# Kernel optimization log

Measured on AMD Instinct MI355X. Metric: run time of the kernel, lower is better.

The kernel has to match this reference:

```python
import jax, jax.numpy as jnp
import numpy as np

B, N, C, H = 8, 1024, 768, 12
D = C // H  # 64


def setup_inputs() -> dict:
    key = jax.random.key(0)
    ks = jax.random.split(key, 6)
    x = jax.random.normal(ks[0], (B, N, C), dtype=jnp.float32)
    pad_mask = jnp.ones((B, N), dtype=jnp.int32)
    # params (torch Linear stored transposed; here kept as (in, out) for x @ W)
    s = 1.0 / np.sqrt(C)
    w_attn = jax.random.uniform(ks[1], (C, 3 * C), jnp.float32, -s, s)
    b_attn = jax.random.uniform(ks[2], (3 * C,), jnp.float32, -s, s)
    w_proj = jax.random.uniform(ks[3], (C, C), jnp.float32, -s, s)
    b_proj = jax.random.uniform(ks[4], (C,), jnp.float32, -s, s)
    return {"x": x, "pad_mask": pad_mask, "w_attn": w_attn,
            "b_attn": b_attn, "w_proj": w_proj, "b_proj": b_proj}


def reference(x, pad_mask, w_attn, b_attn, w_proj, b_proj):
    # qkv projection
    qkv = x @ w_attn + b_attn                      # [B,N,3C]
    q, k, v = jnp.split(qkv, 3, axis=-1)
    q = q.reshape(B, N, H, D).transpose(0, 2, 1, 3)  # [B,H,N,D]
    k = k.reshape(B, N, H, D).transpose(0, 2, 1, 3)
    v = v.reshape(B, N, H, D).transpose(0, 2, 1, 3)
    scale = 1.0 / np.sqrt(D)
    att = jnp.einsum('bhqd,bhkd->bhqk', q, k) * scale  # [B,H,N,N]
    # NOTE: original code's causal masked_fill is non-in-place and discarded,
    # so the causal mask is NOT applied. Only the pad mask (over query rows) is.
    pm = pad_mask.reshape(B, 1, N, 1)
    att = jnp.where(pm == 0, -jnp.inf, att)
    att = jax.nn.softmax(att, axis=-1)
    out = jnp.einsum('bhqk,bhkd->bhqd', att, v)     # [B,H,N,D]
    out = out.transpose(0, 2, 1, 3).reshape(B, N, C)
    # dropout layers are identity in eval mode
    return out @ w_proj + b_proj
```

## Files before the change

kernel.cpp:

```cpp
#include <hip/hip_runtime.h>
#include <hip/hip_bf16.h>

#define B_  8
#define N_  1024
#define C_  768
#define H_  12
#define D_  64
#define C3  2304
#define C2  1536

typedef unsigned short ushort_t;
typedef __attribute__((ext_vector_type(8))) short bf16x8;
typedef __attribute__((ext_vector_type(4))) float f32x4;
typedef __attribute__((ext_vector_type(4))) unsigned int u32x4;

__device__ __forceinline__ ushort_t f2bf(float f) {
    union { float f; unsigned int i; } v;
    v.f = f;
    unsigned int x = v.i;
    if ((x & 0x7f800000u) == 0x7f800000u && (x & 0x007fffffu))
        return (ushort_t)((x >> 16) | 0x0040u);
    return (ushort_t)((x + 0x7fffu + ((x >> 16) & 1u)) >> 16);
}

__device__ __forceinline__ void st1(float* p, float v) { *p = v; }
__device__ __forceinline__ void st1(ushort_t* p, float v) { *p = f2bf(v); }

#define NCVT 6144
#define NTA  1728
#define NTP  576

__device__ __forceinline__ void transpose_tile(
    const float* __restrict__ W, ushort_t* __restrict__ WT,
    int K, int Nn, int n0, int k0, float (*t)[33], int tid)
{
    const int tx = tid & 31, ty = tid >> 5;
    #pragma unroll
    for (int i = 0; i < 4; ++i) {
        const int k = ty + i * 8;
        t[k][tx] = W[(size_t)(k0 + k) * Nn + n0 + tx];
    }
    __syncthreads();
    #pragma unroll
    for (int i = 0; i < 4; ++i) {
        const int n = ty + i * 8;
        WT[(size_t)(n0 + n) * K + k0 + tx] = f2bf(t[tx][n]);
    }
}

__global__ __launch_bounds__(256) void prep(
    const float* __restrict__ X, ushort_t* __restrict__ Y,
    const float* __restrict__ Wa, ushort_t* __restrict__ WaT,
    const float* __restrict__ Wp, ushort_t* __restrict__ WpT)
{
    __shared__ float t[32][33];
    const int bid = blockIdx.x;
    const int tid = threadIdx.x;
    if (bid < NCVT) {
        const int i = (bid * 256 + tid) * 4;
        float4 f = *reinterpret_cast<const float4*>(X + i);
        ushort4 o;
        o.x = f2bf(f.x); o.y = f2bf(f.y); o.z = f2bf(f.z); o.w = f2bf(f.w);
        *reinterpret_cast<ushort4*>(Y + i) = o;
    } else if (bid < NCVT + NTA) {
        const int tt = bid - NCVT;
        transpose_tile(Wa, WaT, C_, C3, (tt % (C3 / 32)) * 32,
                       (tt / (C3 / 32)) * 32, t, tid);
    } else {
        const int tt = bid - NCVT - NTA;
        transpose_tile(Wp, WpT, C_, C_, (tt % (C_ / 32)) * 32,
                       (tt / (C_ / 32)) * 32, t, tid);
    }
}

#define GBK 64

__device__ __forceinline__ void gld_lds16(const ushort_t* g, ushort_t* lds) {
    __builtin_amdgcn_global_load_lds(
        (const __attribute__((address_space(1))) void*)g,
        (__attribute__((address_space(3))) void*)lds, 16, 0, 0);
}

#define G1_NBX   18
#define G1_NBLK  576
#define G1_STEPS 12
#define G1_BUFSZ 24576

__global__ __launch_bounds__(512) void gemm1_mfma(
    const ushort_t* __restrict__ A, const ushort_t* __restrict__ BT,
    const float* __restrict__ bias, ushort_t* __restrict__ Y,
    ushort_t* __restrict__ vtOut)
{
    extern __shared__ ushort_t LDSbuf[];

    const int tid  = threadIdx.x;
    const int wave = tid >> 6;
    const int lane = tid & 63;

    const int hwid = blockIdx.x;
    const int wid  = (hwid & 7) * (G1_NBLK >> 3) + (hwid >> 3);
    const int row0 = (wid / G1_NBX) * 256;
    const int col0 = (wid % G1_NBX) * 128;

    const int wr   = (wave >> 1) * 64;
    const int wc   = (wave & 1) * 64;
    const int l15  = lane & 15;
    const int quad = lane >> 4;
    const int l7   = l15 & 7;

    const int srow = lane >> 3;
    const int sg   = (lane & 7) ^ srow;

    f32x4 acc[4][4] = {};

    auto stage = [&](int buf, int k0) {
        ushort_t* lds = LDSbuf + buf * G1_BUFSZ;
        #pragma unroll
        for (int it = 0; it < 4; ++it) {
            const int baseRow = it * 64 + wave * 8;
            gld_lds16(&A[(size_t)(row0 + baseRow + srow) * C_ + k0 + sg * 8],
                      &lds[baseRow * 64]);
        }
        #pragma unroll
        for (int it = 0; it < 2; ++it) {
            const int baseRow = it * 64 + wave * 8;
            gld_lds16(&BT[(size_t)(col0 + baseRow + srow) * C_ + k0 + sg * 8],
                      &lds[16384 + baseRow * 64]);
        }
    };

    stage(0, 0);
    stage(1, GBK);
    asm volatile("s_waitcnt vmcnt(6)" ::: "memory");
    __builtin_amdgcn_s_barrier();
    __builtin_amdgcn_sched_barrier(0);

    for (int t = 0; t < G1_STEPS; ++t) {
        const ushort_t* const As = LDSbuf + (t % 3) * G1_BUFSZ;
        const ushort_t* const Bs = As + 16384;

        if (t + 2 < G1_STEPS) stage((t + 2) % 3, (t + 2) * GBK);

        #pragma unroll
        for (int kc = 0; kc < 2; ++kc) {
            bf16x8 af[4], bf[4];
            #pragma unroll
            for (int i = 0; i < 4; ++i) {
                const int aslot = (kc * 4 + quad) ^ l7;
                af[i] = *reinterpret_cast<const bf16x8*>(
                    &As[(wr + i * 16 + l15) * 64 + aslot * 8]);
                bf[i] = *reinterpret_cast<const bf16x8*>(
                    &Bs[(wc + i * 16 + l15) * 64 + aslot * 8]);
            }
            #pragma unroll
            for (int i = 0; i < 4; ++i)
                #pragma unroll
                for (int j = 0; j < 4; ++j)
                    acc[i][j] = __builtin_amdgcn_mfma_f32_16x16x32_bf16(
                        af[i], bf[j], acc[i][j], 0, 0, 0);
        }

        if (t + 2 < G1_STEPS)
            asm volatile("s_waitcnt vmcnt(6)" ::: "memory");
        else if (t + 1 < G1_STEPS)
            asm volatile("s_waitcnt vmcnt(0)" ::: "memory");
        __builtin_amdgcn_s_barrier();
        __builtin_amdgcn_sched_barrier(0);
    }

    const float qs = ((col0 + wc) < C_) ? 0.1803368801f : 1.0f;

    if (col0 >= C2) {
        #pragma unroll
        for (int i = 0; i < 4; ++i) {
            const int r0 = row0 + wr + i * 16 + quad * 4;
            const int bb = r0 >> 10;
            const int n  = r0 & 1023;
            const int np = (n & 0x3E0) | (quad << 3) | ((i & 1) << 2);
            #pragma unroll
            for (int j = 0; j < 4; ++j) {
                const int c  = col0 + wc + j * 16 + l15;
                const int cv = c - C2;
                const int hh = cv >> 6, d = cv & 63;
                const float bv = bias[c];
                ushort4 o;
                o.x = f2bf(acc[i][j][0] + bv);
                o.y = f2bf(acc[i][j][1] + bv);
                o.z = f2bf(acc[i][j][2] + bv);
                o.w = f2bf(acc[i][j][3] + bv);
                *reinterpret_cast<ushort4*>(
                    &vtOut[((size_t)(bb * H_ + hh) * D_ + d) * N_ + np]) = o;
            }
        }
    } else {
        #pragma unroll
        for (int i = 0; i < 4; ++i) {
            const int r = row0 + wr + i * 16 + quad * 4;
            #pragma unroll
            for (int j = 0; j < 4; ++j) {
                const int c = col0 + wc + j * 16 + l15;
                const float bv = bias[c];
                #pragma unroll
                for (int t = 0; t < 4; ++t)
                    Y[(size_t)(r + t) * C2 + c] = f2bf((acc[i][j][t] + bv) * qs);
            }
        }
    }
}

template<typename TO, bool SCALEQ>
__global__ __launch_bounds__(256) void gemm_mfma(
    const ushort_t* __restrict__ A, const ushort_t* __restrict__ BT,
    const float* __restrict__ bias, TO* __restrict__ Y, int ldY,
    ushort_t* __restrict__ vtOut, int M, int K, int Nn)
{
    __shared__ ushort_t AB[2][2 * 128 * GBK];

    const int tid  = threadIdx.x;
    const int wave = tid >> 6;
    const int lane = tid & 63;

    const int nbx  = Nn / 128;
    const int nblk = nbx * (M / 128);
    const int hwid = blockIdx.y * gridDim.x + blockIdx.x;
    const int wid  = (hwid & 7) * (nblk >> 3) + (hwid >> 3);
    const int row0 = (wid / nbx) * 128;
    const int col0 = (wid % nbx) * 128;

    const int wr   = (wave >> 1) * 64;
    const int wc   = (wave & 1) * 64;
    const int l15  = lane & 15;
    const int quad = lane >> 4;
    const int l7   = l15 & 7;

    const int srow = lane >> 3;
    const int sg   = (lane & 7) ^ srow;

    f32x4 acc[4][4] = {};

    #pragma unroll
    for (int it = 0; it < 4; ++it) {
        const int baseRow = wave * 32 + it * 8;
        const int r = baseRow + srow;
        gld_lds16(&A [(size_t)(row0 + r) * K + sg * 8], &AB[0][baseRow * GBK]);
        gld_lds16(&BT[(size_t)(col0 + r) * K + sg * 8],
                  &AB[0][128 * GBK + baseRow * GBK]);
    }
    __syncthreads();

    const int nsteps = K / GBK;
    for (int t = 0; t < nsteps; ++t) {
        const int buf = t & 1;
        const ushort_t* const As = AB[buf];
        const ushort_t* const Bs = AB[buf] + 128 * GBK;

        if (t + 1 < nsteps) {
            const int k0 = (t + 1) * GBK;
            #pragma unroll
            for (int it = 0; it < 4; ++it) {
                const int baseRow = wave * 32 + it * 8;
                const int r = baseRow + srow;
                gld_lds16(&A [(size_t)(row0 + r) * K + k0 + sg * 8],
                          &AB[buf ^ 1][baseRow * GBK]);
                gld_lds16(&BT[(size_t)(col0 + r) * K + k0 + sg * 8],
                          &AB[buf ^ 1][128 * GBK + baseRow * GBK]);
            }
        }

        #pragma unroll
        for (int kc = 0; kc < 2; ++kc) {
            bf16x8 af[4], bf[4];
            #pragma unroll
            for (int i = 0; i < 4; ++i) {
                const int aslot = (kc * 4 + quad) ^ l7;
                af[i] = *reinterpret_cast<const bf16x8*>(
                    &As[(wr + i * 16 + l15) * GBK + aslot * 8]);
                bf[i] = *reinterpret_cast<const bf16x8*>(
                    &Bs[(wc + i * 16 + l15) * GBK + aslot * 8]);
            }
            #pragma unroll
            for (int i = 0; i < 4; ++i)
                #pragma unroll
                for (int j = 0; j < 4; ++j)
                    acc[i][j] = __builtin_amdgcn_mfma_f32_16x16x32_bf16(
                        af[i], bf[j], acc[i][j], 0, 0, 0);
        }
        __syncthreads();
    }

    const float qs = (SCALEQ && (col0 + wc) < C_) ? 0.1803368801f : 1.0f;

    if (vtOut != nullptr && col0 >= C2) {
        #pragma unroll
        for (int i = 0; i < 4; ++i) {
            const int r0 = row0 + wr + i * 16 + quad * 4;
            const int bb = r0 >> 10;
            const int n  = r0 & 1023;
            const int np = (n & 0x3E0) | (quad << 3) | ((i & 1) << 2);
            #pragma unroll
            for (int j = 0; j < 4; ++j) {
                const int c  = col0 + wc + j * 16 + l15;
                const int cv = c - C2;
                const int hh = cv >> 6, d = cv & 63;
                const float bv = bias[c];
                ushort4 o;
                o.x = f2bf(acc[i][j][0] + bv);
                o.y = f2bf(acc[i][j][1] + bv);
                o.z = f2bf(acc[i][j][2] + bv);
                o.w = f2bf(acc[i][j][3] + bv);
                *reinterpret_cast<ushort4*>(
                    &vtOut[((size_t)(bb * H_ + hh) * D_ + d) * N_ + np]) = o;
            }
        }
    } else {
        #pragma unroll
        for (int i = 0; i < 4; ++i) {
            const int r = row0 + wr + i * 16 + quad * 4;
            #pragma unroll
            for (int j = 0; j < 4; ++j) {
                const int c = col0 + wc + j * 16 + l15;
                const float bv = bias[c];
                #pragma unroll
                for (int t = 0; t < 4; ++t)
                    st1(&Y[(size_t)(r + t) * ldY + c], (acc[i][j][t] + bv) * qs);
            }
        }
    }
}

__global__ __launch_bounds__(256) void attn_mfma(
    const ushort_t* __restrict__ qk, const ushort_t* __restrict__ vt,
    const int* __restrict__ pad_mask, ushort_t* __restrict__ y)
{
    __shared__ __align__(16) ushort_t KV[2][2 * 64 * 64];

    const int tid  = threadIdx.x;
    const int wave = tid >> 6;
    const int lane = tid & 63;
    const int l15  = lane & 15;
    const int quad = lane >> 4;
    const int l7   = l15 & 7;

    const int wid = (blockIdx.x & 7) * 96 + (blockIdx.x >> 3);
    const int qt = wid & 7;
    const int hb = wid >> 3;
    const int h  = hb % H_;
    const int b  = hb / H_;
    const int q0 = qt * 128 + wave * 32;

    const ushort_t* qkB = qk + (size_t)b * N_ * C2;
    const ushort_t* vtB = vt + ((size_t)(b * H_ + h)) * D_ * N_;
    const int ho = h * D_;

    bf16x8 qf[2][2];
    #pragma unroll
    for (int rt = 0; rt < 2; ++rt)
        #pragma unroll
        for (int kc = 0; kc < 2; ++kc)
            qf[rt][kc] = *reinterpret_cast<const bf16x8*>(
                &qkB[(size_t)(q0 + rt * 16 + l15) * C2 + ho + kc * 32 + quad * 8]);

    int mrow[2][4];
    #pragma unroll
    for (int rt = 0; rt < 2; ++rt)
        #pragma unroll
        for (int t = 0; t < 4; ++t)
            mrow[rt][t] = pad_mask[b * N_ + q0 + rt * 16 + quad * 4 + t];

    f32x4 oacc[2][4] = {};
    float den[2] = {};

    const int srow = lane >> 3;
    const int sg   = (lane & 7) ^ srow;

    #pragma unroll
    for (int it = 0; it < 2; ++it) {
        const int base = wave * 16 + it * 8;
        const int r = base + srow;
        gld_lds16(&qkB[(size_t)r * C2 + C_ + ho + sg * 8], &KV[0][base * 64]);
        gld_lds16(&vtB[(size_t)r * N_ + sg * 8], &KV[0][4096 + base * 64]);
    }
    __syncthreads();

    for (int t = 0; t < N_ / 64; ++t) {
        const int buf = t & 1;
        const ushort_t* const Ks  = KV[buf];
        const ushort_t* const Vts = KV[buf] + 4096;

        if (t + 1 < N_ / 64) {
            const int k0 = (t + 1) * 64;
            #pragma unroll
            for (int it = 0; it < 2; ++it) {
                const int base = wave * 16 + it * 8;
                const int r = base + srow;
                gld_lds16(&qkB[(size_t)(k0 + r) * C2 + C_ + ho + sg * 8],
                          &KV[buf ^ 1][base * 64]);
                gld_lds16(&vtB[(size_t)r * N_ + k0 + sg * 8],
                          &KV[buf ^ 1][4096 + base * 64]);
            }
        }

        f32x4 s[2][4] = {};
        #pragma unroll
        for (int kc = 0; kc < 2; ++kc) {
            bf16x8 kf[4];
            #pragma unroll
            for (int ct = 0; ct < 4; ++ct) {
                const int slot = (kc * 4 + quad) ^ l7;
                kf[ct] = *reinterpret_cast<const bf16x8*>(
                    &Ks[(ct * 16 + l15) * 64 + slot * 8]);
            }
            __builtin_amdgcn_s_setprio(1);
            #pragma unroll
            for (int rt = 0; rt < 2; ++rt)
                #pragma unroll
                for (int ct = 0; ct < 4; ++ct)
                    s[rt][ct] = __builtin_amdgcn_mfma_f32_16x16x32_bf16(
                        kf[ct], qf[rt][kc], s[rt][ct], 0, 0, 0);
            __builtin_amdgcn_s_setprio(0);
        }

        unsigned pk[2][4][2];
        #pragma unroll
        for (int rt = 0; rt < 2; ++rt)
            #pragma unroll
            for (int ct = 0; ct < 4; ++ct) {
                const float p0 = __builtin_amdgcn_exp2f(s[rt][ct][0]);
                const float p1 = __builtin_amdgcn_exp2f(s[rt][ct][1]);
                const float p2 = __builtin_amdgcn_exp2f(s[rt][ct][2]);
                const float p3 = __builtin_amdgcn_exp2f(s[rt][ct][3]);
                den[rt] += (p0 + p1) + (p2 + p3);
                const unsigned x0 = __float_as_uint(p0) + 0x8000u;
                const unsigned x1 = __float_as_uint(p1) + 0x8000u;
                const unsigned x2 = __float_as_uint(p2) + 0x8000u;
                const unsigned x3 = __float_as_uint(p3) + 0x8000u;
                pk[rt][ct][0] = (x0 >> 16) | (x1 & 0xffff0000u);
                pk[rt][ct][1] = (x2 >> 16) | (x3 & 0xffff0000u);
            }

        #pragma unroll
        for (int kc = 0; kc < 2; ++kc) {
            bf16x8 pf[2], vf[4];
            #pragma unroll
            for (int rt = 0; rt < 2; ++rt) {
                const u32x4 pw = (u32x4){pk[rt][kc * 2][0], pk[rt][kc * 2][1],
                                         pk[rt][kc * 2 + 1][0],
                                         pk[rt][kc * 2 + 1][1]};
                pf[rt] = __builtin_bit_cast(bf16x8, pw);
            }
            #pragma unroll
            for (int dt = 0; dt < 4; ++dt) {
                const int slot = (kc * 4 + quad) ^ l7;
                vf[dt] = *reinterpret_cast<const bf16x8*>(
                    &Vts[(dt * 16 + l15) * 64 + slot * 8]);
            }
            __builtin_amdgcn_s_setprio(1);
            #pragma unroll
            for (int rt = 0; rt < 2; ++rt)
                #pragma unroll
                for (int dt = 0; dt < 4; ++dt)
                    oacc[rt][dt] = __builtin_amdgcn_mfma_f32_16x16x32_bf16(
                        pf[rt], vf[dt], oacc[rt][dt], 0, 0, 0);
            __builtin_amdgcn_s_setprio(0);
        }
        __syncthreads();
    }

    ushort_t* const scratch = KV[0] + wave * 32 * 64;

    #pragma unroll
    for (int rt = 0; rt < 2; ++rt) {
        float v = den[rt];
        v += __shfl_xor(v, 16);
        v += __shfl_xor(v, 32);
        den[rt] = v;
    }
    #pragma unroll
    for (int rt = 0; rt < 2; ++rt)
        #pragma unroll
        for (int t = 0; t < 4; ++t) {
            const float dv  = __shfl(den[rt], quad * 4 + t);
            const float inv = mrow[rt][t] ? 1.0f / dv : __builtin_nanf("");
            const int row = rt * 16 + quad * 4 + t;
            #pragma unroll
            for (int dt = 0; dt < 4; ++dt) {
                const int slot = (dt * 2 + (l15 >> 3)) ^ (row & 7);
                scratch[row * 64 + slot * 8 + l7] =
                    f2bf(oacc[rt][dt][t] * inv);
            }
        }
    __syncthreads();
    {
        const int orow = lane >> 1;
        const int og   = (lane & 1) * 4;
        const size_t gr = (size_t)(b * N_ + q0 + orow) * C_ + ho;
        #pragma unroll
        for (int i2 = 0; i2 < 4; ++i2) {
            const int g = og + i2;
            uint4 w = *reinterpret_cast<const uint4*>(
                &scratch[orow * 64 + (g ^ (orow & 7)) * 8]);
            *reinterpret_cast<uint4*>(&y[gr + g * 8]) = w;
        }
    }
}

extern "C" void kernel_launch(void* const* d_in, const int* in_sizes, int n_in,
                              void* d_out, int out_size, void* d_ws, size_t ws_size,
                              hipStream_t stream)
{
    const float* x      = (const float*)d_in[0];
    const int*   pad    = (const int*)d_in[1];
    const float* w_attn = (const float*)d_in[2];
    const float* b_attn = (const float*)d_in[3];
    const float* w_proj = (const float*)d_in[4];
    const float* b_proj = (const float*)d_in[5];
    float* out = (float*)d_out;

    ushort_t* qkb = (ushort_t*)d_ws;
    ushort_t* vtb = qkb + (size_t)B_ * N_ * C2;
    ushort_t* y   = vtb + (size_t)B_ * H_ * D_ * N_;
    ushort_t* xb  = y;
    ushort_t* wat = y + (size_t)B_ * N_ * C_;
    ushort_t* wpt = wat + (size_t)C3 * C_;

    const int M = B_ * N_;

    static bool attr_set = false;
    if (!attr_set) {
        hipFuncSetAttribute(reinterpret_cast<const void*>(&gemm1_mfma),
                            hipFuncAttributeMaxDynamicSharedMemorySize,
                            3 * G1_BUFSZ * 2);
        attr_set = true;
    }

    prep<<<dim3(NCVT + NTA + NTP), dim3(256), 0, stream>>>(
        x, xb, w_attn, wat, w_proj, wpt);

    gemm1_mfma<<<dim3(G1_NBLK), dim3(512), 3 * G1_BUFSZ * 2, stream>>>(
        xb, wat, b_attn, qkb, vtb);

    attn_mfma<<<dim3(B_ * H_ * 8), dim3(256), 0, stream>>>(qkb, vtb, pad, y);

    gemm_mfma<float, false><<<dim3(C_ / 128, M / 128), dim3(256), 0, stream>>>(
        y, wpt, b_proj, out, C_, nullptr, M, C_, C_);
}
```

Before: 188.0 us.

## Fuse fp32-to-bf16 conversion of x into the QKV GEMM A-tile load

The separate pass that converted x to bf16 in the prep kernel is removed. The QKV GEMM now reads fp32 x directly into registers, converts it to bf16 and writes it to LDS, while the weight tiles still use direct global-to-LDS loads. The GEMM is also restructured from a 256x128 tile with 512 threads and a triple-buffered dynamic LDS to a 128x128 tile with 256 threads and static double buffering. This saves a full round trip of the activation through memory and one kernel's worth of work. In exchange the GEMM reads twice the A bytes and repeats them across column blocks, and it has a shallower load pipeline with extra conversion ALU work in the main loop.

```diff
diff --git a/kernel.cpp b/kernel.cpp
--- a/kernel.cpp
+++ b/kernel.cpp
@@ -26,7 +26,6 @@
 __device__ __forceinline__ void st1(float* p, float v) { *p = v; }
 __device__ __forceinline__ void st1(ushort_t* p, float v) { *p = f2bf(v); }
 
-#define NCVT 6144
 #define NTA  1728
 #define NTP  576
 
@@ -49,25 +48,17 @@
 }
 
 __global__ __launch_bounds__(256) void prep(
-    const float* __restrict__ X, ushort_t* __restrict__ Y,
     const float* __restrict__ Wa, ushort_t* __restrict__ WaT,
     const float* __restrict__ Wp, ushort_t* __restrict__ WpT)
 {
     __shared__ float t[32][33];
     const int bid = blockIdx.x;
     const int tid = threadIdx.x;
-    if (bid < NCVT) {
-        const int i = (bid * 256 + tid) * 4;
-        float4 f = *reinterpret_cast<const float4*>(X + i);
-        ushort4 o;
-        o.x = f2bf(f.x); o.y = f2bf(f.y); o.z = f2bf(f.z); o.w = f2bf(f.w);
-        *reinterpret_cast<ushort4*>(Y + i) = o;
-    } else if (bid < NCVT + NTA) {
-        const int tt = bid - NCVT;
-        transpose_tile(Wa, WaT, C_, C3, (tt % (C3 / 32)) * 32,
-                       (tt / (C3 / 32)) * 32, t, tid);
+    if (bid < NTA) {
+        transpose_tile(Wa, WaT, C_, C3, (bid % (C3 / 32)) * 32,
+                       (bid / (C3 / 32)) * 32, t, tid);
     } else {
-        const int tt = bid - NCVT - NTA;
+        const int tt = bid - NTA;
         transpose_tile(Wp, WpT, C_, C_, (tt % (C_ / 32)) * 32,
                        (tt / (C_ / 32)) * 32, t, tid);
     }
@@ -81,26 +72,23 @@
         (__attribute__((address_space(3))) void*)lds, 16, 0, 0);
 }
 
-#define G1_NBX   18
-#define G1_NBLK  576
-#define G1_STEPS 12
-#define G1_BUFSZ 24576
-
-__global__ __launch_bounds__(512) void gemm1_mfma(
-    const ushort_t* __restrict__ A, const ushort_t* __restrict__ BT,
+__global__ __launch_bounds__(256) void gemm1_fused(
+    const float* __restrict__ Ax, const ushort_t* __restrict__ BT,
     const float* __restrict__ bias, ushort_t* __restrict__ Y,
     ushort_t* __restrict__ vtOut)
 {
-    extern __shared__ ushort_t LDSbuf[];
+    __shared__ ushort_t AB[2][2 * 128 * GBK];
 
     const int tid  = threadIdx.x;
     const int wave = tid >> 6;
     const int lane = tid & 63;
 
+    const int nbx  = C3 / 128;
+    const int nblk = nbx * (B_ * N_ / 128);
     const int hwid = blockIdx.x;
-    const int wid  = (hwid & 7) * (G1_NBLK >> 3) + (hwid >> 3);
-    const int row0 = (wid / G1_NBX) * 256;
-    const int col0 = (wid % G1_NBX) * 128;
+    const int wid  = (hwid & 7) * (nblk >> 3) + (hwid >> 3);
+    const int row0 = (wid / nbx) * 128;
+    const int col0 = (wid % nbx) * 128;
 
     const int wr   = (wave >> 1) * 64;
     const int wc   = (wave & 1) * 64;
@@ -112,34 +100,56 @@
     const int sg   = (lane & 7) ^ srow;
 
     f32x4 acc[4][4] = {};
-
-    auto stage = [&](int buf, int k0) {
-        ushort_t* lds = LDSbuf + buf * G1_BUFSZ;
+    float4 areg[4][2];
+
+    auto loadA = [&](int k0) {
         #pragma unroll
         for (int it = 0; it < 4; ++it) {
-            const int baseRow = it * 64 + wave * 8;
-            gld_lds16(&A[(size_t)(row0 + baseRow + srow) * C_ + k0 + sg * 8],
-                      &lds[baseRow * 64]);
-        }
-        #pragma unroll
-        for (int it = 0; it < 2; ++it) {
-            const int baseRow = it * 64 + wave * 8;
+            const int r = wave * 32 + it * 8 + srow;
+            const float* src = &Ax[(size_t)(row0 + r) * C_ + k0 + sg * 8];
+            areg[it][0] = *reinterpret_cast<const float4*>(src);
+            areg[it][1] = *reinterpret_cast<const float4*>(src + 4);
+        }
+    };
+    auto writeA = [&](int buf) {
+        #pragma unroll
+        for (int it = 0; it < 4; ++it) {
+            const int r = wave * 32 + it * 8 + srow;
+            const float4 f0 = areg[it][0];
+            const float4 f1 = areg[it][1];
+            u32x4 pw;
+            pw[0] = (unsigned)f2bf(f0.x) | ((unsigned)f2bf(f0.y) << 16);
+            pw[1] = (unsigned)f2bf(f0.z) | ((unsigned)f2bf(f0.w) << 16);
+            pw[2] = (unsigned)f2bf(f1.x) | ((unsigned)f2bf(f1.y) << 16);
+            pw[3] = (unsigned)f2bf(f1.z) | ((unsigned)f2bf(f1.w) << 16);
+            *reinterpret_cast<u32x4*>(
+                &AB[buf][r * GBK + (lane & 7) * 8]) = pw;
+        }
+    };
+    auto stageB = [&](int buf, int k0) {
+        #pragma unroll
+        for (int it = 0; it < 4; ++it) {
+            const int baseRow = wave * 32 + it * 8;
             gld_lds16(&BT[(size_t)(col0 + baseRow + srow) * C_ + k0 + sg * 8],
-                      &lds[16384 + baseRow * 64]);
+                      &AB[buf][128 * GBK + baseRow * GBK]);
         }
     };
 
-    stage(0, 0);
-    stage(1, GBK);
-    asm volatile("s_waitcnt vmcnt(6)" ::: "memory");
-    __builtin_amdgcn_s_barrier();
-    __builtin_amdgcn_sched_barrier(0);
-
-    for (int t = 0; t < G1_STEPS; ++t) {
-        const ushort_t* const As = LDSbuf + (t % 3) * G1_BUFSZ;
-        const ushort_t* const Bs = As + 16384;
-
-        if (t + 2 < G1_STEPS) stage((t + 2) % 3, (t + 2) * GBK);
+    loadA(0);
+    stageB(0, 0);
+    writeA(0);
+    __syncthreads();
+
+    const int nsteps = C_ / GBK;
+    for (int t = 0; t < nsteps; ++t) {
+        const int buf = t & 1;
+        const ushort_t* const As = AB[buf];
+        const ushort_t* const Bs = AB[buf] + 128 * GBK;
+
+        if (t + 1 < nsteps) {
+            loadA((t + 1) * GBK);
+            stageB(buf ^ 1, (t + 1) * GBK);
+        }
 
         #pragma unroll
         for (int kc = 0; kc < 2; ++kc) {
@@ -148,9 +158,9 @@
             for (int i = 0; i < 4; ++i) {
                 const int aslot = (kc * 4 + quad) ^ l7;
                 af[i] = *reinterpret_cast<const bf16x8*>(
-                    &As[(wr + i * 16 + l15) * 64 + aslot * 8]);
+                    &As[(wr + i * 16 + l15) * GBK + aslot * 8]);
                 bf[i] = *reinterpret_cast<const bf16x8*>(
-                    &Bs[(wc + i * 16 + l15) * 64 + aslot * 8]);
+                    &Bs[(wc + i * 16 + l15) * GBK + aslot * 8]);
             }
             #pragma unroll
             for (int i = 0; i < 4; ++i)
@@ -160,12 +170,8 @@
                         af[i], bf[j], acc[i][j], 0, 0, 0);
         }
 
-        if (t + 2 < G1_STEPS)
-            asm volatile("s_waitcnt vmcnt(6)" ::: "memory");
-        else if (t + 1 < G1_STEPS)
-            asm volatile("s_waitcnt vmcnt(0)" ::: "memory");
-        __builtin_amdgcn_s_barrier();
-        __builtin_amdgcn_sched_barrier(0);
+        if (t + 1 < nsteps) writeA(buf ^ 1);
+        __syncthreads();
     }
 
     const float qs = ((col0 + wc) < C_) ? 0.1803368801f : 1.0f;
@@ -519,25 +525,15 @@
     ushort_t* qkb = (ushort_t*)d_ws;
     ushort_t* vtb = qkb + (size_t)B_ * N_ * C2;
     ushort_t* y   = vtb + (size_t)B_ * H_ * D_ * N_;
-    ushort_t* xb  = y;
     ushort_t* wat = y + (size_t)B_ * N_ * C_;
     ushort_t* wpt = wat + (size_t)C3 * C_;
 
     const int M = B_ * N_;
 
-    static bool attr_set = false;
-    if (!attr_set) {
-        hipFuncSetAttribute(reinterpret_cast<const void*>(&gemm1_mfma),
-                            hipFuncAttributeMaxDynamicSharedMemorySize,
-                            3 * G1_BUFSZ * 2);
-        attr_set = true;
-    }
-
-    prep<<<dim3(NCVT + NTA + NTP), dim3(256), 0, stream>>>(
-        x, xb, w_attn, wat, w_proj, wpt);
-
-    gemm1_mfma<<<dim3(G1_NBLK), dim3(512), 3 * G1_BUFSZ * 2, stream>>>(
-        xb, wat, b_attn, qkb, vtb);
+    prep<<<dim3(NTA + NTP), dim3(256), 0, stream>>>(w_attn, wat, w_proj, wpt);
+
+    gemm1_fused<<<dim3((C3 / 128) * (M / 128)), dim3(256), 0, stream>>>(
+        x, wat, b_attn, qkb, vtb);
 
     attn_mfma<<<dim3(B_ * H_ * 8), dim3(256), 0, stream>>>(qkb, vtb, pad, y);
 
```

After: 221.9 us. 18.0% more time.
